# Performance work log

Measured on AMD Instinct MI355X. Metric: run time of the kernel, lower is better.

## Reference

```python
import jax, jax.numpy as jnp
import numpy as np

B, S, D, K, N = 4, 4096, 768, 24, 8192

def setup_inputs() -> dict:
    key = jax.random.key(0)
    k1, k2, k3, k4 = jax.random.split(key, 4)
    x = jax.random.normal(k1, (B, S, D), dtype=jnp.float32)
    phi = jax.random.normal(k2, (S, K), dtype=jnp.float32)
    M_inputs = jax.random.normal(k3, (D, D), dtype=jnp.float32) / np.sqrt(D)
    M_filters = jax.random.normal(k4, (K, D), dtype=jnp.float32) / np.sqrt(K)
    return {"x": x, "phi": phi, "M_inputs": M_inputs, "M_filters": M_filters, "n": N}


def reference(x, phi, M_inputs, M_filters, n):
    # STU.forward with use_approx=True, use_flash_fft=False
    bsz, sl, d = x.shape
    x_proj = x @ M_inputs               # [B, S, D]
    phi_proj = phi @ M_filters          # [S, D]
    # alternating sign sequence for the 'minus' spectral branch
    sgn = jnp.ones((1, sl, 1), dtype=x.dtype).at[:, 1::2].set(-1.0)
    # filters: [1, S, D, 1] broadcast over the plus/minus stack
    v = phi_proj[None, :, :, None]
    V = jnp.fft.rfft(v, n=n, axis=1)    # [1, n//2+1, D, 1] complex
    U = jnp.stack([x_proj, x_proj * sgn], axis=-1)  # [B, S, D, 2]
    Uf = jnp.fft.rfft(U, n=n, axis=1)   # [B, n//2+1, D, 2]
    U_conv = jnp.fft.irfft(V * Uf, n=n, axis=1)[:, :sl]  # [B, S, D, 2]
    spectral_plus = U_conv[..., 0]
    spectral_minus = U_conv[..., 1] * sgn
    return spectral_plus + spectral_minus
```

## Files before the change

kernel.cpp:

```cpp
#include <hip/hip_runtime.h>
#include <hip/hip_bf16.h>


#define NB 4
#define NS 4096
#define ND 768
#define NK 24

typedef __attribute__((ext_vector_type(8))) short short8;
typedef __attribute__((ext_vector_type(4))) float f32x4;
typedef __attribute__((ext_vector_type(4))) unsigned short u16x4;

static __device__ __forceinline__ float bf2f(unsigned short u) {
  union { unsigned int i; float f; } v; v.i = ((unsigned int)u) << 16; return v.f;
}
static __device__ __forceinline__ unsigned short f2bf(float f) {
  union { float f; unsigned int i; } v; v.f = f;
  return (unsigned short)((v.i + 0x7fffu + ((v.i >> 16) & 1u)) >> 16);
}

__device__ __forceinline__ float2 cadd(float2 a, float2 b){ return make_float2(a.x+b.x, a.y+b.y); }
__device__ __forceinline__ float2 csub(float2 a, float2 b){ return make_float2(a.x-b.x, a.y-b.y); }
__device__ __forceinline__ float2 cmul(float2 a, float2 b){ return make_float2(a.x*b.x-a.y*b.y, a.x*b.y+a.y*b.x); }
__device__ __forceinline__ float2 cmulc(float2 a, float2 b){ return make_float2(a.x*b.x+a.y*b.y, a.y*b.x-a.x*b.y); }

#define C4 0.70710678118654752f
#define C8 0.92387953251128674f
#define S8 0.38268343236508977f
#define TWO_PI 6.28318530717958648f

__device__ __forceinline__ void fft16_dif(float2 v[16]) {
  const float twr[8] = {1.f, C8, C4, S8, 0.f, -S8, -C4, -C8};
  const float twi[8] = {0.f, -S8, -C4, -C8, -1.f, -C8, -C4, -S8};
#pragma unroll
  for (int i = 0; i < 8; ++i) {
    float2 a = v[i], b = v[i+8];
    v[i] = cadd(a, b);
    float2 d = csub(a, b);
    v[i+8] = make_float2(d.x*twr[i]-d.y*twi[i], d.x*twi[i]+d.y*twr[i]);
  }
#pragma unroll
  for (int blk = 0; blk < 16; blk += 8)
#pragma unroll
    for (int i = 0; i < 4; ++i) {
      float2 a = v[blk+i], b = v[blk+i+4];
      v[blk+i] = cadd(a, b);
      float2 d = csub(a, b);
      v[blk+i+4] = make_float2(d.x*twr[2*i]-d.y*twi[2*i], d.x*twi[2*i]+d.y*twr[2*i]);
    }
#pragma unroll
  for (int blk = 0; blk < 16; blk += 4) {
    { float2 a = v[blk],   b = v[blk+2]; v[blk] = cadd(a,b);   v[blk+2] = csub(a,b); }
    { float2 a = v[blk+1], b = v[blk+3]; float2 d = csub(a,b);
      v[blk+1] = cadd(a,b); v[blk+3] = make_float2(d.y, -d.x); }
  }
#pragma unroll
  for (int blk = 0; blk < 16; blk += 2) {
    float2 a = v[blk], b = v[blk+1];
    v[blk] = cadd(a, b); v[blk+1] = csub(a, b);
  }
}

__device__ __forceinline__ void fft16_dif_zero8(float2 v[16]) {
  const float twr[8] = {1.f, C8, C4, S8, 0.f, -S8, -C4, -C8};
  const float twi[8] = {0.f, -S8, -C4, -C8, -1.f, -C8, -C4, -S8};
#pragma unroll
  for (int i = 1; i < 8; ++i) {
    float2 a = v[i];
    v[i+8] = make_float2(a.x*twr[i]-a.y*twi[i], a.x*twi[i]+a.y*twr[i]);
  }
  v[8] = v[0];
#pragma unroll
  for (int blk = 0; blk < 16; blk += 8)
#pragma unroll
    for (int i = 0; i < 4; ++i) {
      float2 a = v[blk+i], b = v[blk+i+4];
      v[blk+i] = cadd(a, b);
      float2 d = csub(a, b);
      v[blk+i+4] = make_float2(d.x*twr[2*i]-d.y*twi[2*i], d.x*twi[2*i]+d.y*twr[2*i]);
    }
#pragma unroll
  for (int blk = 0; blk < 16; blk += 4) {
    { float2 a = v[blk],   b = v[blk+2]; v[blk] = cadd(a,b);   v[blk+2] = csub(a,b); }
    { float2 a = v[blk+1], b = v[blk+3]; float2 d = csub(a,b);
      v[blk+1] = cadd(a,b); v[blk+3] = make_float2(d.y, -d.x); }
  }
#pragma unroll
  for (int blk = 0; blk < 16; blk += 2) {
    float2 a = v[blk], b = v[blk+1];
    v[blk] = cadd(a, b); v[blk+1] = csub(a, b);
  }
}

__device__ __forceinline__ void idft16(float2 v[16]) {
  const float twr[8] = {1.f, C8, C4, S8, 0.f, -S8, -C4, -C8};
  const float twi[8] = {0.f, S8, C4, C8, 1.f, C8, C4, S8};
#pragma unroll
  for (int blk = 0; blk < 16; blk += 2) {
    float2 a = v[blk], b = v[blk+1];
    v[blk] = cadd(a, b); v[blk+1] = csub(a, b);
  }
#pragma unroll
  for (int blk = 0; blk < 16; blk += 4) {
    { float2 a = v[blk],   b = v[blk+2]; v[blk] = cadd(a,b);   v[blk+2] = csub(a,b); }
    { float2 a = v[blk+1], b = v[blk+3]; float2 t = make_float2(-b.y, b.x);
      v[blk+1] = cadd(a,t); v[blk+3] = csub(a,t); }
  }
#pragma unroll
  for (int blk = 0; blk < 16; blk += 8)
#pragma unroll
    for (int i = 0; i < 4; ++i) {
      float2 b = v[blk+i+4];
      float2 t = make_float2(b.x*twr[2*i]-b.y*twi[2*i], b.x*twi[2*i]+b.y*twr[2*i]);
      float2 a = v[blk+i];
      v[blk+i] = cadd(a, t); v[blk+i+4] = csub(a, t);
    }
#pragma unroll
  for (int i = 0; i < 8; ++i) {
    float2 b = v[i+8];
    float2 t = make_float2(b.x*twr[i]-b.y*twi[i], b.x*twi[i]+b.y*twr[i]);
    float2 a = v[i];
    v[i] = cadd(a, t); v[i+8] = csub(a, t);
  }
}

__device__ __forceinline__ void idft16_low8(float2 v[16]) {
  const float twr[8] = {1.f, C8, C4, S8, 0.f, -S8, -C4, -C8};
  const float twi[8] = {0.f, S8, C4, C8, 1.f, C8, C4, S8};
#pragma unroll
  for (int blk = 0; blk < 16; blk += 2) {
    float2 a = v[blk], b = v[blk+1];
    v[blk] = cadd(a, b); v[blk+1] = csub(a, b);
  }
#pragma unroll
  for (int blk = 0; blk < 16; blk += 4) {
    { float2 a = v[blk],   b = v[blk+2]; v[blk] = cadd(a,b);   v[blk+2] = csub(a,b); }
    { float2 a = v[blk+1], b = v[blk+3]; float2 t = make_float2(-b.y, b.x);
      v[blk+1] = cadd(a,t); v[blk+3] = csub(a,t); }
  }
#pragma unroll
  for (int blk = 0; blk < 16; blk += 8)
#pragma unroll
    for (int i = 0; i < 4; ++i) {
      float2 b = v[blk+i+4];
      float2 t = make_float2(b.x*twr[2*i]-b.y*twi[2*i], b.x*twi[2*i]+b.y*twr[2*i]);
      float2 a = v[blk+i];
      v[blk+i] = cadd(a, t); v[blk+i+4] = csub(a, t);
    }
#pragma unroll
  for (int i = 0; i < 8; ++i) {
    float2 b = v[i+8];
    float2 t = make_float2(b.x*twr[i]-b.y*twi[i], b.x*twi[i]+b.y*twr[i]);
    v[i] = cadd(v[i], t);
  }
}

#define BR_TABLE {0,8,4,12,2,10,6,14,1,9,5,13,3,11,7,15}
#define PAD(i) ((i) + ((i) >> 4))

__global__ __launch_bounds__(256) void transpose_cast_Mi(const float* __restrict__ Mi,
                                                         unsigned short* __restrict__ MiT) {
  __shared__ float tile[64][65];
  const int d0 = blockIdx.x * 64;
  const int e0 = blockIdx.y * 64;
  const int tid = threadIdx.x;
#pragma unroll
  for (int i = 0; i < 16; ++i) {
    int ee = (tid >> 6) + i * 4;
    int dd = tid & 63;
    tile[ee][dd] = Mi[(e0 + ee) * ND + d0 + dd];
  }
  __syncthreads();
#pragma unroll
  for (int i = 0; i < 8; ++i) {
    int dd = (tid >> 5) + i * 8;
    int ee2 = (tid & 31) * 2;
    unsigned int w = (unsigned int)f2bf(tile[ee2][dd]) |
                     ((unsigned int)f2bf(tile[ee2 + 1][dd]) << 16);
    *(unsigned int*)(MiT + (size_t)(d0 + dd) * ND + e0 + ee2) = w;
  }
}

__global__ __launch_bounds__(256) void gemm_xprojT(const float* __restrict__ Xf,
                                                   const unsigned short* __restrict__ MiT,
                                                   unsigned short* __restrict__ XPT) {
  __shared__ __align__(16) unsigned char smem[33792];
  unsigned short* As0 = (unsigned short*)smem;
  unsigned short* Bs0 = As0 + 4096;
  unsigned short* As1 = Bs0 + 4096;
  unsigned short* Bs1 = As1 + 4096;

  const int tid = threadIdx.x;
  const int lane = tid & 63;
  const int wave = tid >> 6;
  const int f = blockIdx.x;
  const int swz = (f & 7) * 96 + (f >> 3);
  const int c0 = (swz % 6) * 128;
  const int r0 = (swz / 6) * 128;

  const int rowA = tid >> 2;
  const int colq = (tid & 3) * 8;

  f32x4 acc[4][4];
#pragma unroll
  for (int m = 0; m < 4; ++m)
#pragma unroll
    for (int n = 0; n < 4; ++n) acc[m][n] = (f32x4){0.f, 0.f, 0.f, 0.f};

  {
    const float* ga = Xf + (size_t)(r0 + rowA) * ND + colq;
    float4 p0 = *(const float4*)ga, p1 = *(const float4*)(ga + 4);
    const float* ga2 = ga + (size_t)64 * ND;
    float4 p2 = *(const float4*)ga2, p3 = *(const float4*)(ga2 + 4);
#pragma unroll
    for (int h = 0; h < 2; ++h) {
      int c = wave * 2 + h;
      int rowc = c * 16 + (lane >> 2);
      const unsigned short* gb = MiT + (size_t)(c0 + rowc) * ND + (lane & 3) * 8;
      __builtin_amdgcn_global_load_lds(
          (const __attribute__((address_space(1))) void*)gb,
          (__attribute__((address_space(3))) void*)(Bs0 + c * 512), 16, 0, 0);
    }
    unsigned int w0 = (unsigned int)f2bf(p0.x) | ((unsigned int)f2bf(p0.y) << 16);
    unsigned int w1 = (unsigned int)f2bf(p0.z) | ((unsigned int)f2bf(p0.w) << 16);
    unsigned int w2 = (unsigned int)f2bf(p1.x) | ((unsigned int)f2bf(p1.y) << 16);
    unsigned int w3 = (unsigned int)f2bf(p1.z) | ((unsigned int)f2bf(p1.w) << 16);
    *(uint4*)(As0 + tid * 8) = make_uint4(w0, w1, w2, w3);
    w0 = (unsigned int)f2bf(p2.x) | ((unsigned int)f2bf(p2.y) << 16);
    w1 = (unsigned int)f2bf(p2.z) | ((unsigned int)f2bf(p2.w) << 16);
    w2 = (unsigned int)f2bf(p3.x) | ((unsigned int)f2bf(p3.y) << 16);
    w3 = (unsigned int)f2bf(p3.z) | ((unsigned int)f2bf(p3.w) << 16);
    *(uint4*)(As0 + 2048 + tid * 8) = make_uint4(w0, w1, w2, w3);
  }
  __syncthreads();

  for (int t = 0; t < NK; ++t) {
    unsigned short* Ac = (t & 1) ? As1 : As0;
    unsigned short* Bc = (t & 1) ? Bs1 : Bs0;
    unsigned short* An = (t & 1) ? As0 : As1;
    unsigned short* Bn = (t & 1) ? Bs0 : Bs1;
    const bool pre = (t < NK - 1);
    float4 p0, p1, p2, p3;
    if (pre) {
      const int k0n = (t + 1) * 32;
      const float* ga = Xf + (size_t)(r0 + rowA) * ND + k0n + colq;
      p0 = *(const float4*)ga; p1 = *(const float4*)(ga + 4);
      const float* ga2 = ga + (size_t)64 * ND;
      p2 = *(const float4*)ga2; p3 = *(const float4*)(ga2 + 4);
#pragma unroll
      for (int h = 0; h < 2; ++h) {
        int c = wave * 2 + h;
        int rowc = c * 16 + (lane >> 2);
        const unsigned short* gb = MiT + (size_t)(c0 + rowc) * ND + k0n + (lane & 3) * 8;
        __builtin_amdgcn_global_load_lds(
            (const __attribute__((address_space(1))) void*)gb,
            (__attribute__((address_space(3))) void*)(Bn + c * 512), 16, 0, 0);
      }
    }

    const int wr = (wave >> 1) * 64;
    const int wc = (wave & 1) * 64;
    short8 a[4], b[4];
#pragma unroll
    for (int m = 0; m < 4; ++m)
      a[m] = *(const short8*)(Ac + (wr + m * 16 + (lane & 15)) * 32 + (lane >> 4) * 8);
#pragma unroll
    for (int n = 0; n < 4; ++n)
      b[n] = *(const short8*)(Bc + (wc + n * 16 + (lane & 15)) * 32 + (lane >> 4) * 8);
#pragma unroll
    for (int m = 0; m < 4; ++m)
#pragma unroll
      for (int n = 0; n < 4; ++n)
        acc[m][n] = __builtin_amdgcn_mfma_f32_16x16x32_bf16(a[m], b[n], acc[m][n], 0, 0, 0);

    if (pre) {
      unsigned int w0 = (unsigned int)f2bf(p0.x) | ((unsigned int)f2bf(p0.y) << 16);
      unsigned int w1 = (unsigned int)f2bf(p0.z) | ((unsigned int)f2bf(p0.w) << 16);
      unsigned int w2 = (unsigned int)f2bf(p1.x) | ((unsigned int)f2bf(p1.y) << 16);
      unsigned int w3 = (unsigned int)f2bf(p1.z) | ((unsigned int)f2bf(p1.w) << 16);
      *(uint4*)(An + tid * 8) = make_uint4(w0, w1, w2, w3);
      w0 = (unsigned int)f2bf(p2.x) | ((unsigned int)f2bf(p2.y) << 16);
      w1 = (unsigned int)f2bf(p2.z) | ((unsigned int)f2bf(p2.w) << 16);
      w2 = (unsigned int)f2bf(p3.x) | ((unsigned int)f2bf(p3.y) << 16);
      w3 = (unsigned int)f2bf(p3.z) | ((unsigned int)f2bf(p3.w) << 16);
      *(uint4*)(An + 2048 + tid * 8) = make_uint4(w0, w1, w2, w3);
      __syncthreads();
    }
  }
  __syncthreads();

  unsigned int* Cb = (unsigned int*)smem;
  const int wr = (wave >> 1) * 64;
  const int wc = (wave & 1) * 64;
#pragma unroll
  for (int m = 0; m < 4; ++m)
#pragma unroll
    for (int n = 0; n < 4; ++n) {
      int col = wc + n * 16 + (lane & 15);
      int sp = (wr + m * 16 + (lane >> 4) * 4) >> 1;
      f32x4 a4 = acc[m][n];
      unsigned int w0 = (unsigned int)f2bf(a4[0]) | ((unsigned int)f2bf(a4[1]) << 16);
      unsigned int w1 = (unsigned int)f2bf(a4[2]) | ((unsigned int)f2bf(a4[3]) << 16);
      *(uint2*)(Cb + col * 66 + sp) = make_uint2(w0, w1);
    }
  __syncthreads();
  const int bI = r0 >> 12;
  const int sBase = r0 & (NS - 1);
  {
    int col = tid >> 1, half = tid & 1;
    const unsigned int* srcl = Cb + col * 66 + half * 32;
    unsigned int* dstg = (unsigned int*)(XPT + ((size_t)bI * ND + c0 + col) * NS + sBase) + half * 32;
#pragma unroll
    for (int k = 0; k < 8; ++k)
      *(uint4*)(dstg + k * 4) = *(const uint4*)(srcl + k * 4);
  }
}

__global__ __launch_bounds__(256) void filter_fft(const float* __restrict__ phi,
                                                  const float* __restrict__ Mf,
                                                  float2* __restrict__ Hbr) {
  __shared__ float LR[4352], LI[4352];
  __shared__ float2 TA[256], TB[256];
  const int d = blockIdx.x;
  const int tid = threadIdx.x;
  const int BR[16] = BR_TABLE;
  float2 v[16];

  {
    float sn, cs;
    __sincosf(-(TWO_PI / 4096.f) * (float)tid, &sn, &cs); TA[tid] = make_float2(cs, sn);
    __sincosf(-(TWO_PI / 256.f) * (float)tid, &sn, &cs);  TB[tid] = make_float2(cs, sn);
  }

  float mf[NK];
#pragma unroll
  for (int k = 0; k < NK; ++k) mf[k] = Mf[k * ND + d];
#pragma unroll
  for (int n2 = 0; n2 < 8; ++n2) {
    int m = n2 * 256 + tid;
    const float* pr = phi + (size_t)(2 * m) * NK;
    float acc = 0.f;
#pragma unroll
    for (int k = 0; k < NK; ++k) acc += pr[k] * mf[k];
    v[n2] = make_float2(acc, 0.f);
  }
#pragma unroll
  for (int n2 = 8; n2 < 16; ++n2) v[n2] = make_float2(0.f, 0.f);

  fft16_dif_zero8(v);
  __syncthreads();
  const int t1 = tid >> 4, t0 = tid & 15;
#pragma unroll
  for (int p = 1; p < 16; ++p) v[BR[p]] = cmul(v[BR[p]], cmul(TB[p * t1], TA[p * t0]));
#pragma unroll
  for (int r = 0; r < 16; ++r) { int i = BR[r] * 256 + tid; int s = PAD(i); LR[s] = v[r].x; LI[s] = v[r].y; }
  __syncthreads();

  const int p2 = tid >> 4, n0 = tid & 15;
#pragma unroll
  for (int n1 = 0; n1 < 16; ++n1) { int i = p2 * 256 + n1 * 16 + n0; int s = PAD(i); v[n1] = make_float2(LR[s], LI[s]); }
  fft16_dif(v);
#pragma unroll
  for (int p = 1; p < 16; ++p) v[BR[p]] = cmul(v[BR[p]], TB[p * n0]);
  __syncthreads();
#pragma unroll
  for (int r = 0; r < 16; ++r) { int i = p2 * 256 + BR[r] * 16 + n0; int s = PAD(i); LR[s] = v[r].x; LI[s] = v[r].y; }
  __syncthreads();

#pragma unroll
  for (int q = 0; q < 16; ++q) { int i = tid * 16 + q; int s = PAD(i); v[q] = make_float2(LR[s], LI[s]); }
  fft16_dif(v);
  const float sc = 2.0f / 4096.0f;
  float2* H = Hbr + (size_t)d * 4096;
#pragma unroll
  for (int r = 0; r < 16; ++r)
    H[r * 256 + tid] = make_float2(v[r].x * sc, v[r].y * sc);
}

__global__ __launch_bounds__(256) void conv_kernel(const unsigned short* __restrict__ XPT,
                                                   const float2* __restrict__ Hbr,
                                                   unsigned int* __restrict__ outTb) {
  __shared__ float LR[4352], LI[4352];
  __shared__ float2 TA[256], TB[256];
  const int bd = blockIdx.x;
  const int d = bd % ND;
  const int tid = threadIdx.x;
  const int BR[16] = BR_TABLE;
  float2 v[16];

  {
    float sn, cs;
    __sincosf(-(TWO_PI / 4096.f) * (float)tid, &sn, &cs); TA[tid] = make_float2(cs, sn);
    __sincosf(-(TWO_PI / 256.f) * (float)tid, &sn, &cs);  TB[tid] = make_float2(cs, sn);
  }

  const unsigned int* src = (const unsigned int*)(XPT + (size_t)bd * NS);
#pragma unroll
  for (int n2 = 0; n2 < 8; ++n2) {
    unsigned int w = src[n2 * 256 + tid];
    v[n2] = make_float2(bf2f((unsigned short)(w & 0xffffu)), bf2f((unsigned short)(w >> 16)));
  }
#pragma unroll
  for (int n2 = 8; n2 < 16; ++n2) v[n2] = make_float2(0.f, 0.f);

  fft16_dif_zero8(v);
  __syncthreads();
  const int t1 = tid >> 4, t0 = tid & 15;
#pragma unroll
  for (int p = 1; p < 16; ++p) v[BR[p]] = cmul(v[BR[p]], cmul(TB[p * t1], TA[p * t0]));
#pragma unroll
  for (int r = 0; r < 16; ++r) { int i = BR[r] * 256 + tid; int s = PAD(i); LR[s] = v[r].x; LI[s] = v[r].y; }
  __syncthreads();

  const int p2 = tid >> 4, n0 = tid & 15;
#pragma unroll
  for (int n1 = 0; n1 < 16; ++n1) { int i = p2 * 256 + n1 * 16 + n0; int s = PAD(i); v[n1] = make_float2(LR[s], LI[s]); }
  fft16_dif(v);
#pragma unroll
  for (int p = 1; p < 16; ++p) v[BR[p]] = cmul(v[BR[p]], TB[p * n0]);
  __syncthreads();
#pragma unroll
  for (int r = 0; r < 16; ++r) { int i = p2 * 256 + BR[r] * 16 + n0; int s = PAD(i); LR[s] = v[r].x; LI[s] = v[r].y; }
  __syncthreads();

#pragma unroll
  for (int q = 0; q < 16; ++q) { int i = tid * 16 + q; int s = PAD(i); v[q] = make_float2(LR[s], LI[s]); }
  fft16_dif(v);
  const float2* H = Hbr + (size_t)d * 4096;
#pragma unroll
  for (int r = 0; r < 16; ++r) v[r] = cmul(v[r], H[r * 256 + tid]);
  idft16(v);
#pragma unroll
  for (int n = 1; n < 16; ++n) v[n] = cmulc(v[n], TB[n * (tid & 15)]);
#pragma unroll
  for (int n = 0; n < 16; ++n) { int i = tid * 16 + n; int s = PAD(i); LR[s] = v[n].x; LI[s] = v[n].y; }
  __syncthreads();

#pragma unroll
  for (int r = 0; r < 16; ++r) { int i = p2 * 256 + BR[r] * 16 + n0; int s = PAD(i); v[r] = make_float2(LR[s], LI[s]); }
  idft16(v);
  {
    float2 cA = TA[p2 * n0];
#pragma unroll
    for (int n = 0; n < 16; ++n) v[n] = cmulc(v[n], cmul(TB[p2 * n], cA));
  }
  __syncthreads();
#pragma unroll
  for (int n = 0; n < 16; ++n) { int i = p2 * 256 + n * 16 + n0; int s = PAD(i); LR[s] = v[n].x; LI[s] = v[n].y; }
  __syncthreads();

#pragma unroll
  for (int r = 0; r < 16; ++r) { int i = BR[r] * 256 + tid; int s = PAD(i); v[r] = make_float2(LR[s], LI[s]); }
  idft16_low8(v);
  unsigned int* dst = outTb + (size_t)bd * 2048;
#pragma unroll
  for (int n2 = 0; n2 < 8; ++n2) {
    float2 y = v[n2];
    unsigned int w = (unsigned int)f2bf(y.x) | ((unsigned int)f2bf(y.y) << 16);
    dst[(n2 << 8) + tid] = w;
  }
}

__global__ __launch_bounds__(256) void transpose_out(const unsigned int* __restrict__ outTb,
                                                     float* __restrict__ out) {
  __shared__ float tile[64][65];
  const int b = blockIdx.z;
  const int d0 = blockIdx.y * 64;
  const int s0 = blockIdx.x * 64;
  const int tid = threadIdx.x;
#pragma unroll
  for (int i = 0; i < 8; ++i) {
    int dd = (tid >> 5) + i * 8;
    int ss2 = (tid & 31) * 2;
    unsigned int w = outTb[(((size_t)b * ND + d0 + dd) * NS + s0 + ss2) >> 1];
    tile[dd][ss2]     = bf2f((unsigned short)(w & 0xffffu));
    tile[dd][ss2 + 1] = bf2f((unsigned short)(w >> 16));
  }
  __syncthreads();
#pragma unroll
  for (int i = 0; i < 16; ++i) {
    int ss = (tid >> 6) + i * 4;
    int dd = tid & 63;
    out[((size_t)b * NS + s0 + ss) * ND + d0 + dd] = tile[dd][ss];
  }
}

extern "C" void kernel_launch(void* const* d_in, const int* in_sizes, int n_in,
                              void* d_out, int out_size, void* d_ws, size_t ws_size,
                              hipStream_t stream) {
  const float* x   = (const float*)d_in[0];
  const float* phi = (const float*)d_in[1];
  const float* Mi  = (const float*)d_in[2];
  const float* Mf  = (const float*)d_in[3];
  float* out = (float*)d_out;

  const size_t SZ_XPT = (size_t)NB * ND * NS * 2;
  const size_t SZ_HBR = (size_t)ND * 4096 * 8;
  const size_t SZ_POOL = (size_t)NB * ND * NS * 4;
  if (ws_size < SZ_XPT + SZ_HBR + SZ_POOL) return;

  char* ws = (char*)d_ws;
  unsigned short* xprojT = (unsigned short*)ws;
  float2* Hbr = (float2*)(ws + SZ_XPT);
  char* pool = ws + SZ_XPT + SZ_HBR;
  unsigned int* outTb = (unsigned int*)pool;
  unsigned short* MiT = (unsigned short*)(pool + 25165824);

  transpose_cast_Mi<<<dim3(ND / 64, ND / 64), 256, 0, stream>>>(Mi, MiT);
  gemm_xprojT<<<768, 256, 0, stream>>>(x, MiT, xprojT);
  filter_fft<<<ND, 256, 0, stream>>>(phi, Mf, Hbr);
  conv_kernel<<<NB * ND, 256, 0, stream>>>(xprojT, Hbr, outTb);
  transpose_out<<<dim3(NS / 64, ND / 64, NB), 256, 0, stream>>>(outTb, out);
}
```

Measured before the change: 126.2 us.

## Triple-buffer x-projection GEMM with two-stage-ahead prefetch and partial waitcnts

The x@M_inputs GEMM mainloop moves from double to triple LDS buffering. Global loads are issued two k-steps ahead, and the pipeline is driven by manual vmcnt and lgkmcnt waits around a raw s_barrier instead of __syncthreads. Two register sets alternate for the fp32 A tile, so the bf16 conversion of one step overlaps the loads of the next. This is meant to hide global memory latency better, at the cost of 48KB of LDS per block (which may reduce occupancy) and fragile hand-written waitcnt ordering.

Result: slower. 137.6 us (+9.0%).

```diff
diff --git a/kernel.cpp b/kernel.cpp
--- a/kernel.cpp
+++ b/kernel.cpp
@@ -181,15 +181,65 @@
   }
 }
 
+#define GEMM_ISSUE(T, LDRG)                                                    \
+  {                                                                            \
+    const int nxt = ((T) + 2) % 3;                                             \
+    const int k0n = ((T) + 2) * 32;                                            \
+    const float* ga = Xf + (size_t)(r0 + rowA) * ND + k0n + colq;              \
+    LDRG[0] = *(const float4*)ga; LDRG[1] = *(const float4*)(ga + 4);          \
+    const float* ga2 = ga + (size_t)64 * ND;                                   \
+    LDRG[2] = *(const float4*)ga2; LDRG[3] = *(const float4*)(ga2 + 4);        \
+    unsigned short* Bn = (unsigned short*)(smem + nxt * 16384) + 4096;         \
+    _Pragma("unroll")                                                          \
+    for (int h = 0; h < 2; ++h) {                                              \
+      int c = wave * 2 + h;                                                    \
+      int rowc = c * 16 + (lane >> 2);                                         \
+      const unsigned short* gb = MiT + (size_t)(c0 + rowc) * ND + k0n + (lane & 3) * 8; \
+      __builtin_amdgcn_global_load_lds(                                        \
+          (const __attribute__((address_space(1))) void*)gb,                   \
+          (__attribute__((address_space(3))) void*)(Bn + c * 512), 16, 0, 0);  \
+    }                                                                          \
+  }
+
+#define GEMM_COMPUTE(T)                                                        \
+  {                                                                            \
+    const int cur = (T) % 3;                                                   \
+    unsigned short* Ac = (unsigned short*)(smem + cur * 16384);                \
+    unsigned short* Bc = Ac + 4096;                                            \
+    short8 a[4], b[4];                                                         \
+    _Pragma("unroll")                                                          \
+    for (int m = 0; m < 4; ++m)                                                \
+      a[m] = *(const short8*)(Ac + (wr + m * 16 + (lane & 15)) * 32 + (lane >> 4) * 8); \
+    _Pragma("unroll")                                                          \
+    for (int n = 0; n < 4; ++n)                                                \
+      b[n] = *(const short8*)(Bc + (wc + n * 16 + (lane & 15)) * 32 + (lane >> 4) * 8); \
+    _Pragma("unroll")                                                          \
+    for (int m = 0; m < 4; ++m)                                                \
+      _Pragma("unroll")                                                        \
+      for (int n = 0; n < 4; ++n)                                              \
+        acc[m][n] = __builtin_amdgcn_mfma_f32_16x16x32_bf16(a[m], b[n], acc[m][n], 0, 0, 0); \
+  }
+
+#define GEMM_PACK(T, PKRG)                                                     \
+  {                                                                            \
+    const int pkb = ((T) + 1) % 3;                                             \
+    unsigned short* An = (unsigned short*)(smem + pkb * 16384);                \
+    unsigned int w0 = (unsigned int)f2bf(PKRG[0].x) | ((unsigned int)f2bf(PKRG[0].y) << 16); \
+    unsigned int w1 = (unsigned int)f2bf(PKRG[0].z) | ((unsigned int)f2bf(PKRG[0].w) << 16); \
+    unsigned int w2 = (unsigned int)f2bf(PKRG[1].x) | ((unsigned int)f2bf(PKRG[1].y) << 16); \
+    unsigned int w3 = (unsigned int)f2bf(PKRG[1].z) | ((unsigned int)f2bf(PKRG[1].w) << 16); \
+    *(uint4*)(An + tid * 8) = make_uint4(w0, w1, w2, w3);                      \
+    w0 = (unsigned int)f2bf(PKRG[2].x) | ((unsigned int)f2bf(PKRG[2].y) << 16); \
+    w1 = (unsigned int)f2bf(PKRG[2].z) | ((unsigned int)f2bf(PKRG[2].w) << 16); \
+    w2 = (unsigned int)f2bf(PKRG[3].x) | ((unsigned int)f2bf(PKRG[3].y) << 16); \
+    w3 = (unsigned int)f2bf(PKRG[3].z) | ((unsigned int)f2bf(PKRG[3].w) << 16); \
+    *(uint4*)(An + 2048 + tid * 8) = make_uint4(w0, w1, w2, w3);               \
+  }
+
 __global__ __launch_bounds__(256) void gemm_xprojT(const float* __restrict__ Xf,
                                                    const unsigned short* __restrict__ MiT,
                                                    unsigned short* __restrict__ XPT) {
-  __shared__ __align__(16) unsigned char smem[33792];
-  unsigned short* As0 = (unsigned short*)smem;
-  unsigned short* Bs0 = As0 + 4096;
-  unsigned short* As1 = Bs0 + 4096;
-  unsigned short* Bs1 = As1 + 4096;
-
+  __shared__ __align__(16) unsigned char smem[49152];
   const int tid = threadIdx.x;
   const int lane = tid & 63;
   const int wave = tid >> 6;
@@ -200,18 +250,23 @@
 
   const int rowA = tid >> 2;
   const int colq = (tid & 3) * 8;
+  const int wr = (wave >> 1) * 64;
+  const int wc = (wave & 1) * 64;
 
   f32x4 acc[4][4];
 #pragma unroll
   for (int m = 0; m < 4; ++m)
 #pragma unroll
     for (int n = 0; n < 4; ++n) acc[m][n] = (f32x4){0.f, 0.f, 0.f, 0.f};
+
+  float4 pA[4], pB[4];
 
   {
     const float* ga = Xf + (size_t)(r0 + rowA) * ND + colq;
-    float4 p0 = *(const float4*)ga, p1 = *(const float4*)(ga + 4);
+    float4 q0 = *(const float4*)ga, q1 = *(const float4*)(ga + 4);
     const float* ga2 = ga + (size_t)64 * ND;
-    float4 p2 = *(const float4*)ga2, p3 = *(const float4*)(ga2 + 4);
+    float4 q2 = *(const float4*)ga2, q3 = *(const float4*)(ga2 + 4);
+    unsigned short* B0 = (unsigned short*)(smem) + 4096;
 #pragma unroll
     for (int h = 0; h < 2; ++h) {
       int c = wave * 2 + h;
@@ -219,79 +274,69 @@
       const unsigned short* gb = MiT + (size_t)(c0 + rowc) * ND + (lane & 3) * 8;
       __builtin_amdgcn_global_load_lds(
           (const __attribute__((address_space(1))) void*)gb,
-          (__attribute__((address_space(3))) void*)(Bs0 + c * 512), 16, 0, 0);
-    }
-    unsigned int w0 = (unsigned int)f2bf(p0.x) | ((unsigned int)f2bf(p0.y) << 16);
-    unsigned int w1 = (unsigned int)f2bf(p0.z) | ((unsigned int)f2bf(p0.w) << 16);
-    unsigned int w2 = (unsigned int)f2bf(p1.x) | ((unsigned int)f2bf(p1.y) << 16);
-    unsigned int w3 = (unsigned int)f2bf(p1.z) | ((unsigned int)f2bf(p1.w) << 16);
-    *(uint4*)(As0 + tid * 8) = make_uint4(w0, w1, w2, w3);
-    w0 = (unsigned int)f2bf(p2.x) | ((unsigned int)f2bf(p2.y) << 16);
-    w1 = (unsigned int)f2bf(p2.z) | ((unsigned int)f2bf(p2.w) << 16);
-    w2 = (unsigned int)f2bf(p3.x) | ((unsigned int)f2bf(p3.y) << 16);
-    w3 = (unsigned int)f2bf(p3.z) | ((unsigned int)f2bf(p3.w) << 16);
-    *(uint4*)(As0 + 2048 + tid * 8) = make_uint4(w0, w1, w2, w3);
-  }
-  __syncthreads();
-
-  for (int t = 0; t < NK; ++t) {
-    unsigned short* Ac = (t & 1) ? As1 : As0;
-    unsigned short* Bc = (t & 1) ? Bs1 : Bs0;
-    unsigned short* An = (t & 1) ? As0 : As1;
-    unsigned short* Bn = (t & 1) ? Bs0 : Bs1;
-    const bool pre = (t < NK - 1);
-    float4 p0, p1, p2, p3;
-    if (pre) {
-      const int k0n = (t + 1) * 32;
-      const float* ga = Xf + (size_t)(r0 + rowA) * ND + k0n + colq;
-      p0 = *(const float4*)ga; p1 = *(const float4*)(ga + 4);
-      const float* ga2 = ga + (size_t)64 * ND;
-      p2 = *(const float4*)ga2; p3 = *(const float4*)(ga2 + 4);
-#pragma unroll
-      for (int h = 0; h < 2; ++h) {
-        int c = wave * 2 + h;
-        int rowc = c * 16 + (lane >> 2);
-        const unsigned short* gb = MiT + (size_t)(c0 + rowc) * ND + k0n + (lane & 3) * 8;
-        __builtin_amdgcn_global_load_lds(
-            (const __attribute__((address_space(1))) void*)gb,
-            (__attribute__((address_space(3))) void*)(Bn + c * 512), 16, 0, 0);
-      }
-    }
-
-    const int wr = (wave >> 1) * 64;
-    const int wc = (wave & 1) * 64;
-    short8 a[4], b[4];
-#pragma unroll
-    for (int m = 0; m < 4; ++m)
-      a[m] = *(const short8*)(Ac + (wr + m * 16 + (lane & 15)) * 32 + (lane >> 4) * 8);
-#pragma unroll
-    for (int n = 0; n < 4; ++n)
-      b[n] = *(const short8*)(Bc + (wc + n * 16 + (lane & 15)) * 32 + (lane >> 4) * 8);
-#pragma unroll
-    for (int m = 0; m < 4; ++m)
-#pragma unroll
-      for (int n = 0; n < 4; ++n)
-        acc[m][n] = __builtin_amdgcn_mfma_f32_16x16x32_bf16(a[m], b[n], acc[m][n], 0, 0, 0);
-
-    if (pre) {
-      unsigned int w0 = (unsigned int)f2bf(p0.x) | ((unsigned int)f2bf(p0.y) << 16);
-      unsigned int w1 = (unsigned int)f2bf(p0.z) | ((unsigned int)f2bf(p0.w) << 16);
-      unsigned int w2 = (unsigned int)f2bf(p1.x) | ((unsigned int)f2bf(p1.y) << 16);
-      unsigned int w3 = (unsigned int)f2bf(p1.z) | ((unsigned int)f2bf(p1.w) << 16);
+          (__attribute__((address_space(3))) void*)(B0 + c * 512), 16, 0, 0);
+    }
+    {
+      unsigned short* An = (unsigned short*)smem;
+      unsigned int w0 = (unsigned int)f2bf(q0.x) | ((unsigned int)f2bf(q0.y) << 16);
+      unsigned int w1 = (unsigned int)f2bf(q0.z) | ((unsigned int)f2bf(q0.w) << 16);
+      unsigned int w2 = (unsigned int)f2bf(q1.x) | ((unsigned int)f2bf(q1.y) << 16);
+      unsigned int w3 = (unsigned int)f2bf(q1.z) | ((unsigned int)f2bf(q1.w) << 16);
       *(uint4*)(An + tid * 8) = make_uint4(w0, w1, w2, w3);
-      w0 = (unsigned int)f2bf(p2.x) | ((unsigned int)f2bf(p2.y) << 16);
-      w1 = (unsigned int)f2bf(p2.z) | ((unsigned int)f2bf(p2.w) << 16);
-      w2 = (unsigned int)f2bf(p3.x) | ((unsigned int)f2bf(p3.y) << 16);
-      w3 = (unsigned int)f2bf(p3.z) | ((unsigned int)f2bf(p3.w) << 16);
+      w0 = (unsigned int)f2bf(q2.x) | ((unsigned int)f2bf(q2.y) << 16);
+      w1 = (unsigned int)f2bf(q2.z) | ((unsigned int)f2bf(q2.w) << 16);
+      w2 = (unsigned int)f2bf(q3.x) | ((unsigned int)f2bf(q3.y) << 16);
+      w3 = (unsigned int)f2bf(q3.z) | ((unsigned int)f2bf(q3.w) << 16);
       *(uint4*)(An + 2048 + tid * 8) = make_uint4(w0, w1, w2, w3);
-      __syncthreads();
-    }
-  }
+    }
+    const float* gb1 = Xf + (size_t)(r0 + rowA) * ND + 32 + colq;
+    pB[0] = *(const float4*)gb1; pB[1] = *(const float4*)(gb1 + 4);
+    const float* gb2 = gb1 + (size_t)64 * ND;
+    pB[2] = *(const float4*)gb2; pB[3] = *(const float4*)(gb2 + 4);
+    unsigned short* B1 = (unsigned short*)(smem + 16384) + 4096;
+#pragma unroll
+    for (int h = 0; h < 2; ++h) {
+      int c = wave * 2 + h;
+      int rowc = c * 16 + (lane >> 2);
+      const unsigned short* gb = MiT + (size_t)(c0 + rowc) * ND + 32 + (lane & 3) * 8;
+      __builtin_amdgcn_global_load_lds(
+          (const __attribute__((address_space(1))) void*)gb,
+          (__attribute__((address_space(3))) void*)(B1 + c * 512), 16, 0, 0);
+    }
+    asm volatile("s_waitcnt vmcnt(6)" ::: "memory");
+    asm volatile("s_waitcnt lgkmcnt(0)" ::: "memory");
+    __builtin_amdgcn_s_barrier();
+    asm volatile("" ::: "memory");
+  }
+
+  for (int tt = 0; tt < 22; tt += 2) {
+    GEMM_ISSUE(tt, pA);
+    GEMM_COMPUTE(tt);
+    asm volatile("s_waitcnt vmcnt(6)" ::: "memory");
+    GEMM_PACK(tt, pB);
+    asm volatile("s_waitcnt lgkmcnt(0)" ::: "memory");
+    __builtin_amdgcn_s_barrier();
+    asm volatile("" ::: "memory");
+
+    GEMM_ISSUE(tt + 1, pB);
+    GEMM_COMPUTE(tt + 1);
+    asm volatile("s_waitcnt vmcnt(6)" ::: "memory");
+    GEMM_PACK(tt + 1, pA);
+    asm volatile("s_waitcnt lgkmcnt(0)" ::: "memory");
+    __builtin_amdgcn_s_barrier();
+    asm volatile("" ::: "memory");
+  }
+  GEMM_COMPUTE(22);
+  asm volatile("s_waitcnt vmcnt(0)" ::: "memory");
+  GEMM_PACK(22, pB);
+  asm volatile("s_waitcnt lgkmcnt(0)" ::: "memory");
+  __builtin_amdgcn_s_barrier();
+  asm volatile("" ::: "memory");
+  GEMM_COMPUTE(23);
+
   __syncthreads();
 
   unsigned int* Cb = (unsigned int*)smem;
-  const int wr = (wave >> 1) * 64;
-  const int wc = (wave & 1) * 64;
 #pragma unroll
   for (int m = 0; m < 4; ++m)
 #pragma unroll
```
